# Performance work log

Measured on AMD Instinct MI355X. Metric: run time of the kernel, lower is better.

## Reference

```python
import jax, jax.numpy as jnp
import numpy as np

EMB, NW, H, L, FF, VOCAB, BS = 512, 64, 8, 4, 2048, 50257, 16


def setup_inputs() -> dict:
    key = jax.random.key(0)
    ks = jax.random.split(key, 8)
    d = EMB
    def n(k, shape, s=0.02):
        return jax.random.normal(k, shape, jnp.float32) * s
    return {
        "w_emb": jax.random.normal(ks[0], (BS, NW, d), jnp.float32),
        "table": jax.random.normal(ks[1], (VOCAB, d), jnp.float32) * 0.02,
        "word_enc": n(ks[2], (NW + 1, d)),            # learned token encodings
        "Wqkv": n(ks[3], (L, 3 * d, d)),              # in_proj per layer
        "bqkv": jnp.zeros((L, 3 * d), jnp.float32),
        "Wo": n(ks[4], (L, d, d)),
        "bo": jnp.zeros((L, d), jnp.float32),
        "W1": n(ks[5], (L, FF, d)),
        "b1": jnp.zeros((L, FF), jnp.float32),
        "W2": n(ks[6], (L, d, FF)),
        "b2": jnp.zeros((L, d), jnp.float32),
        "g1": jnp.ones((L, d), jnp.float32),
        "be1": jnp.zeros((L, d), jnp.float32),
        "g2": jnp.ones((L, d), jnp.float32),
        "be2": jnp.zeros((L, d), jnp.float32),
    }


def _ln(x, g, b, eps=1e-5):
    m = x.mean(-1, keepdims=True)
    v = ((x - m) ** 2).mean(-1, keepdims=True)
    return (x - m) * jax.lax.rsqrt(v + eps) * g + b


def reference(w_emb, table, word_enc, Wqkv, bqkv, Wo, bo, W1, b1, W2, b2, g1, be1, g2, be2):
    bs, _, d = w_emb.shape
    dh = d // H
    scale = 1.0 / np.sqrt(dh).astype(np.float32)
    # prepend zero token, add learned encodings -> (bs, NW+1, d)
    x = jnp.concatenate([jnp.zeros((bs, 1, d), w_emb.dtype), w_emb], axis=1) + word_enc
    for l in range(L):
        # self-attention (post-LN TransformerEncoderLayer, ReLU FFN)
        qkv = x @ Wqkv[l].T + bqkv[l]
        q, k, v = jnp.split(qkv, 3, axis=-1)
        s = x.shape[1]
        q = q.reshape(bs, s, H, dh)
        k = k.reshape(bs, s, H, dh)
        v = v.reshape(bs, s, H, dh)
        att = jax.nn.softmax(jnp.einsum('bqhd,bkhd->bhqk', q, k) * scale, axis=-1)
        ctx = jnp.einsum('bhqk,bkhd->bqhd', att, v).reshape(bs, s, d)
        x = _ln(x + ctx @ Wo[l].T + bo[l], g1[l], be1[l])
        h = jax.nn.relu(x @ W1[l].T + b1[l])
        x = _ln(x + h @ W2[l].T + b2[l], g2[l], be2[l])
    out = x[:, :-1]                                   # drop last position -> (bs, NW, d)
    # linear lookup: (out * table).sum(-1) == out @ table.T
    return jnp.einsum('bnd,vd->bnv', out, table)
```

## Files before the change

kernel.cpp:

```cpp
#include <hip/hip_runtime.h>
#include <hip/hip_bf16.h>

#define EMB 512
#define NW  64
#define SEQ 65
#define NH  8
#define DH  64
#define NL  4
#define FF_ 2048
#define VOCAB 50257
#define BS  16
#define TOK (BS*SEQ)
#define TOUT (BS*NW)

typedef short short8  __attribute__((ext_vector_type(8)));
typedef unsigned short ushort8n __attribute__((ext_vector_type(8)));
typedef float f32x4   __attribute__((ext_vector_type(4)));

__device__ __forceinline__ unsigned short f2bf(float f) {
    unsigned u = __float_as_uint(f);
    return (unsigned short)((u + 0x7FFF + ((u >> 16) & 1)) >> 16);
}

template<int N> __device__ __forceinline__ void wait_vm() {
    asm volatile("s_waitcnt vmcnt(%0)" :: "n"(N) : "memory");
}

constexpr int ilog2c(int v) { return v == 32 ? 5 : v == 64 ? 6 : v == 128 ? 7 : 0; }

#define SZ_WQKV (NL*3*EMB*EMB)
#define SZ_WO   (NL*EMB*EMB)
#define SZ_W1   (NL*FF_*EMB)
#define SZ_W2   (NL*EMB*FF_)
#define SZ_TAB  (VOCAB*EMB)
#define CVT_TOTAL (SZ_WQKV+SZ_WO+SZ_W1+SZ_W2+SZ_TAB)
#define O_WO   (SZ_WQKV)
#define O_W1   (O_WO+SZ_WO)
#define O_W2   (O_W1+SZ_W1)
#define O_TAB  (O_W2+SZ_W2)

__global__ void cvt_kernel(const float* __restrict__ wqkv, const float* __restrict__ wo,
                           const float* __restrict__ w1, const float* __restrict__ w2,
                           const float* __restrict__ table, unsigned short* __restrict__ dst) {
    const int U = CVT_TOTAL / 8;
    for (int u = blockIdx.x * blockDim.x + threadIdx.x; u < U; u += gridDim.x * blockDim.x) {
        size_t elem = (size_t)u * 8;
        const float* src; size_t loc = elem;
        if      (elem < O_WO)  { src = wqkv; }
        else if (elem < O_W1)  { src = wo;    loc = elem - O_WO; }
        else if (elem < O_W2)  { src = w1;    loc = elem - O_W1; }
        else if (elem < O_TAB) { src = w2;    loc = elem - O_W2; }
        else                   { src = table; loc = elem - O_TAB; }
        float4 f0 = *(const float4*)(src + loc);
        float4 f1 = *(const float4*)(src + loc + 4);
        ushort8n o;
        o[0]=f2bf(f0.x); o[1]=f2bf(f0.y); o[2]=f2bf(f0.z); o[3]=f2bf(f0.w);
        o[4]=f2bf(f1.x); o[5]=f2bf(f1.y); o[6]=f2bf(f1.z); o[7]=f2bf(f1.w);
        *(ushort8n*)(dst + elem) = o;
    }
}

__global__ void embed_kernel(const float* __restrict__ w_emb,
                             const float* __restrict__ word_enc,
                             float* __restrict__ x32,
                             unsigned short* __restrict__ x16) {
    int idx = blockIdx.x * blockDim.x + threadIdx.x;
    const int total = BS * SEQ * EMB;
    if (idx >= total) return;
    int d = idx & (EMB - 1);
    int s = (idx >> 9) % SEQ;
    int b = idx / (SEQ * EMB);
    float we = word_enc[s * EMB + d];
    float e = (s == 0) ? 0.f : w_emb[((size_t)b * NW + (s - 1)) * EMB + d];
    float v = e + we;
    x32[idx] = v;
    x16[idx] = f2bf(v);
}

template<int TM, int TN, int BK, int OUT_BF16, int RELU, int COMPACT, int SPLITK>
__global__ __launch_bounds__(256) void gemm4(const unsigned short* __restrict__ A,
                                             const unsigned short* __restrict__ B,
                                             const float* __restrict__ bias,
                                             void* __restrict__ C0,
                                             void* __restrict__ C1,
                                             const float* __restrict__ res,
                                             int M, int N, int K, int lda, int ldb) {
    constexpr int LTM = ilog2c(TM);
    constexpr int LTN = ilog2c(TN);
    constexpr int FR  = TM / 32, FC = TN / 32;
    constexpr int WRH = TM / 2,  WCH = TN / 2;
    constexpr int KCH = BK / 32;
    constexpr int AI  = (TM * BK) / (8 * 256);
    constexpr int BI  = (TN * BK) / (8 * 256);
    constexpr int L   = AI + BI;
    constexpr int ASZ = TM * BK * 2;
    constexpr int STRIDE = (TM + TN) * BK * 2;
    __shared__ __align__(16) char smem[3 * STRIDE];

    int t = threadIdx.x;
    int w = t >> 6, l = t & 63;
    int wr = w >> 1, wc = w & 1;
    int lr = l & 15, lh = l >> 4;

    int mtiles = (M + TM - 1) / TM;
    int ntiles = (N + TN - 1) / TN;
    int bid = blockIdx.x;
    int nchunk = gridDim.x >> 3;
    int lin = (bid & 7) * nchunk + (bid >> 3);
    int part = 0;
    if (SPLITK) { int tpp = mtiles * ntiles; part = (lin >= tpp); lin -= part * tpp; }
    int m0 = (lin % mtiles) * TM;
    int n0 = (lin / mtiles) * TN;

    const unsigned short* Ap = A + (size_t)part * K;
    const unsigned short* Bp = B + (size_t)part * K;
    float* Cf = (float*)(part ? C1 : C0);
    const float* biasp = (SPLITK && part) ? nullptr : bias;
    const float* resp  = (SPLITK && part) ? nullptr : res;

    f32x4 acc[FR][FC] = {};
    const int nt = K / BK;

    auto stageA = [&](int kt, int p) {
        char* dst = smem + p * STRIDE;
        #pragma unroll
        for (int i = 0; i < AI; ++i) {
            int tt = i * 256 + t;
            int row = tt & (TM - 1);
            int slot = tt >> LTM;
            int gr = m0 + row;
            if (COMPACT) gr = ((gr >> 6) * SEQ) + (gr & 63);
            else if (gr >= M) gr = M - 1;
            const unsigned short* gp = Ap + (size_t)gr * lda + kt + slot * 8;
            __builtin_amdgcn_global_load_lds(
                (const __attribute__((address_space(1))) void*)gp,
                (__attribute__((address_space(3))) void*)(dst + (size_t)(i * 256 + w * 64) * 16),
                16, 0, 0);
        }
    };
    auto stageB = [&](int kt, int p) {
        char* dst = smem + p * STRIDE + ASZ;
        #pragma unroll
        for (int i = 0; i < BI; ++i) {
            int tt = i * 256 + t;
            int row = tt & (TN - 1);
            int slot = tt >> LTN;
            int gr = n0 + row;
            if (gr >= N) gr = N - 1;
            const unsigned short* gp = Bp + (size_t)gr * ldb + kt + slot * 8;
            __builtin_amdgcn_global_load_lds(
                (const __attribute__((address_space(1))) void*)gp,
                (__attribute__((address_space(3))) void*)(dst + (size_t)(i * 256 + w * 64) * 16),
                16, 0, 0);
        }
    };
    auto compute = [&](int p) {
        const unsigned short* as_ = (const unsigned short*)(smem + p * STRIDE);
        const unsigned short* bs_ = as_ + TM * BK;
        #pragma unroll
        for (int kk = 0; kk < KCH; ++kk) {
            short8 af[FR], bfv[FC];
            #pragma unroll
            for (int mi = 0; mi < FR; ++mi)
                af[mi] = *(const short8*)(as_ + ((size_t)(kk * 4 + lh) * TM + wr * WRH + mi * 16 + lr) * 8);
            #pragma unroll
            for (int ni = 0; ni < FC; ++ni)
                bfv[ni] = *(const short8*)(bs_ + ((size_t)(kk * 4 + lh) * TN + wc * WCH + ni * 16 + lr) * 8);
            #pragma unroll
            for (int mi = 0; mi < FR; ++mi)
                #pragma unroll
                for (int ni = 0; ni < FC; ++ni)
                    acc[mi][ni] = __builtin_amdgcn_mfma_f32_16x16x32_bf16(af[mi], bfv[ni], acc[mi][ni], 0, 0, 0);
        }
    };

    stageA(0, 0); stageB(0, 0);
    if (nt > 1) { stageA(BK, 1); stageB(BK, 1); }

    for (int it = 0; it < nt; ++it) {
        if (it + 1 < nt) wait_vm<L>(); else wait_vm<0>();
        __builtin_amdgcn_s_barrier();
        __builtin_amdgcn_sched_barrier(0);
        if (it + 2 < nt) {
            stageA((it + 2) * BK, (it + 2) % 3);
            stageB((it + 2) * BK, (it + 2) % 3);
        }
        __builtin_amdgcn_s_setprio(1);
        compute(it % 3);
        __builtin_amdgcn_s_setprio(0);
        __builtin_amdgcn_sched_barrier(0);
    }

    if (OUT_BF16) {
        #pragma unroll
        for (int ni = 0; ni < FC; ++ni) {
            int gcol = n0 + wc * WCH + ni * 16 + lr;
            if (gcol >= N) continue;
            float bv = biasp ? biasp[gcol] : 0.f;
            #pragma unroll
            for (int mi = 0; mi < FR; ++mi)
                #pragma unroll
                for (int r = 0; r < 4; ++r) {
                    int grow = m0 + wr * WRH + mi * 16 + lh * 4 + r;
                    if (grow >= M) continue;
                    float v = acc[mi][ni][r] + bv;
                    if (RELU) v = fmaxf(v, 0.f);
                    ((unsigned short*)C0)[(size_t)grow * N + gcol] = f2bf(v);
                }
        }
    } else {
        __syncthreads();
        constexpr int PAD = WCH + 4;
        constexpr int CPR = WCH / 4;
        constexpr int J   = (16 * CPR) / 64;
        float* ep = (float*)smem + (size_t)w * 16 * PAD;
        #pragma unroll
        for (int mi = 0; mi < FR; ++mi) {
            asm volatile("s_waitcnt lgkmcnt(0)" ::: "memory");
            __builtin_amdgcn_sched_barrier(0);
            #pragma unroll
            for (int ni = 0; ni < FC; ++ni)
                #pragma unroll
                for (int r = 0; r < 4; ++r)
                    ep[(lh * 4 + r) * PAD + ni * 16 + lr] = acc[mi][ni][r];
            asm volatile("s_waitcnt lgkmcnt(0)" ::: "memory");
            __builtin_amdgcn_sched_barrier(0);
            #pragma unroll
            for (int j = 0; j < J; ++j) {
                int f4  = j * 64 + l;
                int row = f4 / CPR;
                int c4  = f4 % CPR;
                int grow = m0 + wr * WRH + mi * 16 + row;
                int gc   = n0 + wc * WCH + c4 * 4;
                if (grow < M) {
                    float4 v = *(const float4*)(ep + row * PAD + c4 * 4);
                    if (gc + 3 < N) {
                        if (biasp) {
                            float4 b4 = *(const float4*)(biasp + gc);
                            v.x += b4.x; v.y += b4.y; v.z += b4.z; v.w += b4.w;
                        }
                        if (resp) {
                            const float* rp = resp + (size_t)grow * N + gc;
                            v.x += rp[0]; v.y += rp[1]; v.z += rp[2]; v.w += rp[3];
                        }
                        if (RELU) {
                            v.x = fmaxf(v.x, 0.f); v.y = fmaxf(v.y, 0.f);
                            v.z = fmaxf(v.z, 0.f); v.w = fmaxf(v.w, 0.f);
                        }
                        *(float4*)(Cf + (size_t)grow * N + gc) = v;
                    } else {
                        const float* pv = (const float*)&v;
                        #pragma unroll
                        for (int e = 0; e < 4; ++e)
                            if (gc + e < N) {
                                float vv = pv[e];
                                if (biasp) vv += biasp[gc + e];
                                if (resp)  vv += resp[(size_t)grow * N + gc + e];
                                if (RELU)  vv = fmaxf(vv, 0.f);
                                Cf[(size_t)grow * N + gc + e] = vv;
                            }
                    }
                }
            }
        }
    }
}

template<int TM, int TN, int OUT_BF16, int RELU, int COMPACT>
__global__ __launch_bounds__(256) void gemm2(const unsigned short* __restrict__ A,
                                             const float* __restrict__ B,
                                             const float* __restrict__ bias,
                                             void* __restrict__ C,
                                             int M, int N, int K) {
    constexpr int LTM = (TM == 128) ? 7 : 6;
    constexpr int FR  = TM / 32, FC = TN / 32;
    constexpr int WRH = TM / 2,  WCH = TN / 2;
    constexpr int AI  = TM / 64;
    constexpr int TPR = 256 / TN;
    constexpr int SPT = 4 / TPR;
    constexpr int STRIDE = (TM + TN) * 64;
    __shared__ __align__(16) char smem[2 * STRIDE];

    int t = threadIdx.x;
    int w = t >> 6, l = t & 63;
    int wr = w >> 1, wc = w & 1;
    int lr = l & 15, lh = l >> 4;
    int m0 = blockIdx.y * TM, n0 = blockIdx.x * TN;

    int br = t / TPR, bh = t % TPR;
    int gbr = n0 + br; if (gbr >= N) gbr = N - 1;
    const float* bbase = B + (size_t)gbr * K + bh * (SPT * 8);

    f32x4  acc[FR][FC] = {};
    float4 breg[TN / 32];
    const int nt = K >> 5;

    auto stageA = [&](int kt, int p) {
        char* dst = smem + p * STRIDE;
        #pragma unroll
        for (int i = 0; i < AI; ++i) {
            int tt   = i * 256 + t;
            int row  = tt & (TM - 1);
            int slot = tt >> LTM;
            int gr   = m0 + row;
            if (COMPACT) gr = ((gr >> 6) * SEQ) + (gr & 63);
            else if (gr >= M) gr = M - 1;
            const unsigned short* gp = A + (size_t)gr * K + kt + slot * 8;
            __builtin_amdgcn_global_load_lds(
                (const __attribute__((address_space(1))) void*)gp,
                (__attribute__((address_space(3))) void*)(dst + (size_t)(i * 256 + w * 64) * 16),
                16, 0, 0);
        }
    };
    auto loadB = [&](int kt) {
        const float* bp = bbase + kt;
        #pragma unroll
        for (int j = 0; j < TN / 32; ++j) breg[j] = *(const float4*)(bp + j * 4);
    };
    auto writeB = [&](int p) {
        unsigned short* bs = (unsigned short*)(smem + p * STRIDE + TM * 64);
        #pragma unroll
        for (int s = 0; s < SPT; ++s) {
            ushort8n u;
            #pragma unroll
            for (int e = 0; e < 8; ++e) {
                float f = ((const float*)&breg[s * 2 + (e >> 2)])[e & 3];
                u[e] = f2bf(f);
            }
            int slot = bh * SPT + s;
            *(ushort8n*)(bs + ((size_t)slot * TN + br) * 8) = u;
        }
    };
    auto compute = [&](int p) {
        const unsigned short* as_ = (const unsigned short*)(smem + p * STRIDE);
        const unsigned short* bs_ = as_ + TM * 32;
        short8 af[FR], bfv[FC];
        #pragma unroll
        for (int mi = 0; mi < FR; ++mi)
            af[mi] = *(const short8*)(as_ + ((size_t)lh * TM + wr * WRH + mi * 16 + lr) * 8);
        #pragma unroll
        for (int ni = 0; ni < FC; ++ni)
            bfv[ni] = *(const short8*)(bs_ + ((size_t)lh * TN + wc * WCH + ni * 16 + lr) * 8);
        #pragma unroll
        for (int mi = 0; mi < FR; ++mi)
            #pragma unroll
            for (int ni = 0; ni < FC; ++ni)
                acc[mi][ni] = __builtin_amdgcn_mfma_f32_16x16x32_bf16(af[mi], bfv[ni], acc[mi][ni], 0, 0, 0);
    };

    stageA(0, 0); loadB(0); writeB(0);
    __syncthreads();
    for (int it = 0; it < nt; ++it) {
        int p = it & 1;
        if (it + 1 < nt) { stageA((it + 1) << 5, 1 - p); loadB((it + 1) << 5); }
        compute(p);
        if (it + 1 < nt) writeB(1 - p);
        __syncthreads();
    }

    #pragma unroll
    for (int ni = 0; ni < FC; ++ni) {
        int gcol = n0 + wc * WCH + ni * 16 + lr;
        if (gcol >= N) continue;
        float bv = bias ? bias[gcol] : 0.f;
        #pragma unroll
        for (int mi = 0; mi < FR; ++mi)
            #pragma unroll
            for (int r = 0; r < 4; ++r) {
                int grow = m0 + wr * WRH + mi * 16 + lh * 4 + r;
                if (grow >= M) continue;
                float v = acc[mi][ni][r] + bv;
                if (RELU) v = fmaxf(v, 0.f);
                if (OUT_BF16) ((unsigned short*)C)[(size_t)grow * N + gcol] = f2bf(v);
                else          ((float*)C)[(size_t)grow * N + gcol] = v;
            }
    }
}

#define APAD 65
__global__ __launch_bounds__(256) void attn_fused(const float* __restrict__ qkv,
                                                  unsigned short* __restrict__ ctx16) {
    int qpart = blockIdx.x;
    int h = blockIdx.y, b = blockIdx.z;
    __shared__ float Ks[SEQ * APAD];
    __shared__ float Vs[SEQ * APAD];
    __shared__ float qsh[4][64];
    __shared__ float pws[4][SEQ + 3];

    const float* base = qkv + (size_t)b * SEQ * (3 * EMB) + h * DH;
    int t = threadIdx.x;
    for (int idx = t; idx < SEQ * 16; idx += 256) {
        int r = idx >> 4, c4 = (idx & 15) << 2;
        const float* rp = base + (size_t)r * (3 * EMB);
        float4 kv = *(const float4*)(rp + EMB + c4);
        float4 vv = *(const float4*)(rp + 2 * EMB + c4);
        float* kd = Ks + r * APAD + c4;
        kd[0] = kv.x; kd[1] = kv.y; kd[2] = kv.z; kd[3] = kv.w;
        float* vd = Vs + r * APAD + c4;
        vd[0] = vv.x; vd[1] = vv.y; vd[2] = vv.z; vd[3] = vv.w;
    }
    __syncthreads();

    int w = t >> 6, l = t & 63;
    int qstart = qpart ? 33 : 0;
    int qend   = qpart ? SEQ : 33;
    for (int qi = qstart + w; qi < qend; qi += 4) {
        qsh[w][l] = base[(size_t)qi * (3 * EMB) + l];
        float s = 0.f;
        #pragma unroll 16
        for (int d = 0; d < DH; ++d) s += qsh[w][d] * Ks[l * APAD + d];
        s *= 0.125f;
        float s64 = -1e30f;
        if (l == 0) {
            float acc64 = 0.f;
            #pragma unroll 16
            for (int d = 0; d < DH; ++d) acc64 += qsh[w][d] * Ks[64 * APAD + d];
            s64 = acc64 * 0.125f;
        }
        float m = (l == 0) ? fmaxf(s, s64) : s;
        #pragma unroll
        for (int off = 32; off >= 1; off >>= 1) m = fmaxf(m, __shfl_xor(m, off));
        float e = __expf(s - m);
        pws[w][l] = e;
        float esum = e;
        if (l == 0) { float e64 = __expf(s64 - m); pws[w][64] = e64; esum += e64; }
        #pragma unroll
        for (int off = 32; off >= 1; off >>= 1) esum += __shfl_xor(esum, off);
        float inv = 1.f / esum;
        float acc = 0.f;
        #pragma unroll 13
        for (int j = 0; j < SEQ; ++j) acc += pws[w][j] * Vs[j * APAD + l];
        ctx16[((size_t)b * SEQ + qi) * EMB + h * DH + l] = f2bf(acc * inv);
    }
}

__global__ __launch_bounds__(128) void ln_kernel(const float* __restrict__ x,
                                                 const float* __restrict__ p,
                                                 const float* __restrict__ g,
                                                 const float* __restrict__ be,
                                                 float* __restrict__ y32,
                                                 unsigned short* __restrict__ y16) {
    int row = blockIdx.x;
    int t = threadIdx.x;
    const float4 xv = ((const float4*)(x + (size_t)row * EMB))[t];
    const float4 pv = ((const float4*)(p + (size_t)row * EMB))[t];
    float v0 = xv.x + pv.x, v1 = xv.y + pv.y, v2 = xv.z + pv.z, v3 = xv.w + pv.w;
    float sum = v0 + v1 + v2 + v3;
    float sq  = v0 * v0 + v1 * v1 + v2 * v2 + v3 * v3;
    #pragma unroll
    for (int off = 32; off >= 1; off >>= 1) {
        sum += __shfl_down(sum, off);
        sq  += __shfl_down(sq,  off);
    }
    __shared__ float s0[2], s1[2];
    if ((t & 63) == 0) { s0[t >> 6] = sum; s1[t >> 6] = sq; }
    __syncthreads();
    float S = s0[0] + s0[1], Q = s1[0] + s1[1];
    float mean = S * (1.f / EMB);
    float var  = Q * (1.f / EMB) - mean * mean;
    float rstd = rsqrtf(var + 1e-5f);
    const float4 gv = ((const float4*)g)[t];
    const float4 bv = ((const float4*)be)[t];
    float4 o;
    o.x = (v0 - mean) * rstd * gv.x + bv.x;
    o.y = (v1 - mean) * rstd * gv.y + bv.y;
    o.z = (v2 - mean) * rstd * gv.z + bv.z;
    o.w = (v3 - mean) * rstd * gv.w + bv.w;
    ((float4*)(y32 + (size_t)row * EMB))[t] = o;
    ushort4 h;
    h.x = f2bf(o.x); h.y = f2bf(o.y); h.z = f2bf(o.z); h.w = f2bf(o.w);
    ((ushort4*)(y16 + (size_t)row * EMB))[t] = h;
}

extern "C" void kernel_launch(void* const* d_in, const int* in_sizes, int n_in,
                              void* d_out, int out_size, void* d_ws, size_t ws_size,
                              hipStream_t stream) {
    const float* w_emb    = (const float*)d_in[0];
    const float* table    = (const float*)d_in[1];
    const float* word_enc = (const float*)d_in[2];
    const float* Wqkv     = (const float*)d_in[3];
    const float* bqkv     = (const float*)d_in[4];
    const float* Wo       = (const float*)d_in[5];
    const float* bo       = (const float*)d_in[6];
    const float* W1       = (const float*)d_in[7];
    const float* b1       = (const float*)d_in[8];
    const float* W2       = (const float*)d_in[9];
    const float* b2       = (const float*)d_in[10];
    const float* g1       = (const float*)d_in[11];
    const float* be1      = (const float*)d_in[12];
    const float* g2       = (const float*)d_in[13];
    const float* be2      = (const float*)d_in[14];
    float* out = (float*)d_out;

    const size_t act_bytes = (size_t)TOK * EMB * 4 * 3
                           + (size_t)TOK * 3 * EMB * 4
                           + (size_t)TOK * EMB * 2 * 3
                           + (size_t)TOK * FF_ * 2;
    const size_t wgt_bytes = (size_t)CVT_TOTAL * 2;
    const bool fast = ws_size >= act_bytes + wgt_bytes;

    char* ws = (char*)d_ws;
    unsigned short* wgt16 = nullptr;
    if (fast) { wgt16 = (unsigned short*)ws; ws += wgt_bytes; }
    float* xa32  = (float*)ws;                    ws += (size_t)TOK * EMB * 4;
    float* xb32  = (float*)ws;                    ws += (size_t)TOK * EMB * 4;
    float* qkv32 = (float*)ws;                    ws += (size_t)TOK * 3 * EMB * 4;
    float* proj32= (float*)ws;                    ws += (size_t)TOK * EMB * 4;
    unsigned short* hbuf16= (unsigned short*)ws;  ws += (size_t)TOK * FF_ * 2;
    unsigned short* xa16  = (unsigned short*)ws;  ws += (size_t)TOK * EMB * 2;
    unsigned short* xb16  = (unsigned short*)ws;  ws += (size_t)TOK * EMB * 2;
    unsigned short* ctx16 = (unsigned short*)ws;  ws += (size_t)TOK * EMB * 2;
    float* projb  = qkv32;

    if (fast) cvt_kernel<<<2048, 256, 0, stream>>>(Wqkv, Wo, W1, W2, table, wgt16);

    {
        int total = BS * SEQ * EMB;
        embed_kernel<<<(total + 255) / 256, 256, 0, stream>>>(w_emb, word_enc, xa32, xa16);
    }

    if (fast) {
        const unsigned short* wq16 = wgt16;
        const unsigned short* wo16 = wgt16 + O_WO;
        const unsigned short* w116 = wgt16 + O_W1;
        const unsigned short* w216 = wgt16 + O_W2;
        const unsigned short* tab16= wgt16 + O_TAB;

        for (int l = 0; l < NL; ++l) {
            gemm4<64,32,64,0,0,0,0><<<dim3(816), 256, 0, stream>>>(
                xa16, wq16 + (size_t)l * 3 * EMB * EMB, bqkv + (size_t)l * 3 * EMB,
                qkv32, nullptr, nullptr, TOK, 3 * EMB, EMB, EMB, EMB);
            attn_fused<<<dim3(2, NH, BS), 256, 0, stream>>>(qkv32, ctx16);
            gemm4<64,32,64,0,0,0,1><<<dim3(544), 256, 0, stream>>>(
                ctx16, wo16 + (size_t)l * EMB * EMB, bo + (size_t)l * EMB,
                proj32, projb, xa32, TOK, EMB, 256, EMB, EMB);
            ln_kernel<<<TOK, 128, 0, stream>>>(proj32, projb,
                g1 + (size_t)l * EMB, be1 + (size_t)l * EMB, xb32, xb16);
            gemm4<64,32,64,1,1,0,0><<<dim3(1088), 256, 0, stream>>>(
                xb16, w116 + (size_t)l * FF_ * EMB, b1 + (size_t)l * FF_,
                hbuf16, nullptr, nullptr, TOK, FF_, EMB, EMB, EMB);
            gemm4<64,32,64,0,0,0,1><<<dim3(544), 256, 0, stream>>>(
                hbuf16, w216 + (size_t)l * EMB * FF_, b2 + (size_t)l * EMB,
                proj32, projb, xb32, TOK, EMB, 1024, FF_, FF_);
            ln_kernel<<<TOK, 128, 0, stream>>>(proj32, projb,
                g2 + (size_t)l * EMB, be2 + (size_t)l * EMB, xa32, xa16);
        }
        gemm4<64,128,32,0,0,1,0><<<dim3(6288), 256, 0, stream>>>(
            xa16, tab16, nullptr, out, nullptr, nullptr, TOUT, VOCAB, EMB, EMB, EMB);
    } else {
        for (int l = 0; l < NL; ++l) {
            const float* Wqkv_l = Wqkv + (size_t)l * 3 * EMB * EMB;
            const float* Wo_l   = Wo   + (size_t)l * EMB * EMB;
            const float* W1_l   = W1   + (size_t)l * FF_ * EMB;
            const float* W2_l   = W2   + (size_t)l * EMB * FF_;
            gemm2<64,64,0,0,0><<<dim3((3 * EMB) / 64, (TOK + 63) / 64), 256, 0, stream>>>(
                xa16, Wqkv_l, bqkv + (size_t)l * 3 * EMB, qkv32, TOK, 3 * EMB, EMB);
            attn_fused<<<dim3(2, NH, BS), 256, 0, stream>>>(qkv32, ctx16);
            gemm2<64,64,0,0,0><<<dim3(EMB / 64, (TOK + 63) / 64), 256, 0, stream>>>(
                ctx16, Wo_l, bo + (size_t)l * EMB, proj32, TOK, EMB, EMB);
            ln_kernel<<<TOK, 128, 0, stream>>>(xa32, proj32, g1 + (size_t)l * EMB, be1 + (size_t)l * EMB, xb32, xb16);
            gemm2<64,64,1,1,0><<<dim3(FF_ / 64, (TOK + 63) / 64), 256, 0, stream>>>(
                xb16, W1_l, b1 + (size_t)l * FF_, hbuf16, TOK, FF_, EMB);
            gemm2<64,64,0,0,0><<<dim3(EMB / 64, (TOK + 63) / 64), 256, 0, stream>>>(
                hbuf16, W2_l, b2 + (size_t)l * EMB, proj32, TOK, EMB, FF_);
            ln_kernel<<<TOK, 128, 0, stream>>>(xb32, proj32, g2 + (size_t)l * EMB, be2 + (size_t)l * EMB, xa32, xa16);
        }
        gemm2<128,128,0,0,1><<<dim3((VOCAB + 127) / 128, TOUT / 128), 256, 0, stream>>>(
            xa16, table, nullptr, out, TOUT, VOCAB, EMB);
    }
}
```

Measured before the change: 575.5 us.

## Fuse layer GEMMs with bias/residual/LayerNorm via direct-load full-row dgemm

```diff
diff --git a/kernel.cpp b/kernel.cpp
--- a/kernel.cpp
+++ b/kernel.cpp
@@ -12,6 +12,7 @@
 #define BS  16
 #define TOK (BS*SEQ)
 #define TOUT (BS*NW)
+#define MT32 ((TOK + 31) / 32)
 
 typedef short short8  __attribute__((ext_vector_type(8)));
 typedef unsigned short ushort8n __attribute__((ext_vector_type(8)));
@@ -77,14 +78,147 @@
     x16[idx] = f2bf(v);
 }
 
-template<int TM, int TN, int BK, int OUT_BF16, int RELU, int COMPACT, int SPLITK>
+template<int K, int MODE>
+__global__ __launch_bounds__(512) void dgemm(const unsigned short* __restrict__ A,
+                                             const unsigned short* __restrict__ B,
+                                             const float* __restrict__ bias,
+                                             const float* __restrict__ res,
+                                             const float* __restrict__ g,
+                                             const float* __restrict__ be,
+                                             float* __restrict__ out32,
+                                             unsigned short* __restrict__ out16,
+                                             int M, int N) {
+    int t = threadIdx.x, w = t >> 6, l = t & 63;
+    int lr = l & 15, lh = l >> 4;
+    int bid = blockIdx.x;
+    int mt = bid % MT32, ns = bid / MT32;
+    int m0 = mt * 32;
+    int c0 = ns * 512 + w * 64;
+
+    int ar0 = m0 + lr;       if (ar0 >= M) ar0 = M - 1;
+    int ar1 = m0 + 16 + lr;  if (ar1 >= M) ar1 = M - 1;
+    const unsigned short* a0 = A + (size_t)ar0 * K + lh * 8;
+    const unsigned short* a1 = A + (size_t)ar1 * K + lh * 8;
+    const unsigned short* bb = B + (size_t)(c0 + lr) * K + lh * 8;
+
+    f32x4 acc[2][4] = {};
+    #pragma unroll 2
+    for (int k0 = 0; k0 < K; k0 += 32) {
+        short8 af0 = *(const short8*)(a0 + k0);
+        short8 af1 = *(const short8*)(a1 + k0);
+        short8 bfv[4];
+        #pragma unroll
+        for (int ni = 0; ni < 4; ++ni)
+            bfv[ni] = *(const short8*)(bb + (size_t)ni * 16 * K + k0);
+        #pragma unroll
+        for (int ni = 0; ni < 4; ++ni) {
+            acc[0][ni] = __builtin_amdgcn_mfma_f32_16x16x32_bf16(af0, bfv[ni], acc[0][ni], 0, 0, 0);
+            acc[1][ni] = __builtin_amdgcn_mfma_f32_16x16x32_bf16(af1, bfv[ni], acc[1][ni], 0, 0, 0);
+        }
+    }
+
+    if (MODE == 2) {
+        __shared__ float sred[32][8], qred[32][8], mstat[32], rstat[32];
+        float vals[2][4][4];
+        float bv[4];
+        #pragma unroll
+        for (int ni = 0; ni < 4; ++ni) bv[ni] = bias[c0 + ni * 16 + lr];
+        float ps[2][4] = {}, pq[2][4] = {};
+        #pragma unroll
+        for (int mi = 0; mi < 2; ++mi)
+            #pragma unroll
+            for (int r = 0; r < 4; ++r) {
+                int row = m0 + mi * 16 + lh * 4 + r;
+                int rc = row < M ? row : M - 1;
+                #pragma unroll
+                for (int ni = 0; ni < 4; ++ni) {
+                    float v = acc[mi][ni][r] + bv[ni] + res[(size_t)rc * 512 + c0 + ni * 16 + lr];
+                    vals[mi][ni][r] = v;
+                    ps[mi][r] += v;
+                    pq[mi][r] += v * v;
+                }
+            }
+        #pragma unroll
+        for (int off = 8; off >= 1; off >>= 1)
+            #pragma unroll
+            for (int mi = 0; mi < 2; ++mi)
+                #pragma unroll
+                for (int r = 0; r < 4; ++r) {
+                    ps[mi][r] += __shfl_xor(ps[mi][r], off);
+                    pq[mi][r] += __shfl_xor(pq[mi][r], off);
+                }
+        if (lr == 0) {
+            #pragma unroll
+            for (int mi = 0; mi < 2; ++mi)
+                #pragma unroll
+                for (int r = 0; r < 4; ++r) {
+                    sred[mi * 16 + lh * 4 + r][w] = ps[mi][r];
+                    qred[mi * 16 + lh * 4 + r][w] = pq[mi][r];
+                }
+        }
+        __syncthreads();
+        if (t < 32) {
+            float S = 0.f, Q = 0.f;
+            #pragma unroll
+            for (int j = 0; j < 8; ++j) { S += sred[t][j]; Q += qred[t][j]; }
+            float mean = S * (1.f / 512.f);
+            float var  = Q * (1.f / 512.f) - mean * mean;
+            mstat[t] = mean;
+            rstat[t] = rsqrtf(var + 1e-5f);
+        }
+        __syncthreads();
+        float gv[4], bev[4];
+        #pragma unroll
+        for (int ni = 0; ni < 4; ++ni) {
+            gv[ni] = g[c0 + ni * 16 + lr];
+            bev[ni] = be[c0 + ni * 16 + lr];
+        }
+        #pragma unroll
+        for (int mi = 0; mi < 2; ++mi)
+            #pragma unroll
+            for (int r = 0; r < 4; ++r) {
+                int lrow = mi * 16 + lh * 4 + r;
+                int row = m0 + lrow;
+                if (row >= M) continue;
+                float mean = mstat[lrow], rstd = rstat[lrow];
+                #pragma unroll
+                for (int ni = 0; ni < 4; ++ni) {
+                    int col = c0 + ni * 16 + lr;
+                    float o = (vals[mi][ni][r] - mean) * rstd * gv[ni] + bev[ni];
+                    out32[(size_t)row * 512 + col] = o;
+                    out16[(size_t)row * 512 + col] = f2bf(o);
+                }
+            }
+    } else {
+        float bv[4];
+        #pragma unroll
+        for (int ni = 0; ni < 4; ++ni) bv[ni] = bias ? bias[c0 + ni * 16 + lr] : 0.f;
+        #pragma unroll
+        for (int mi = 0; mi < 2; ++mi)
+            #pragma unroll
+            for (int r = 0; r < 4; ++r) {
+                int row = m0 + mi * 16 + lh * 4 + r;
+                if (row >= M) continue;
+                #pragma unroll
+                for (int ni = 0; ni < 4; ++ni) {
+                    int col = c0 + ni * 16 + lr;
+                    float v = acc[mi][ni][r] + bv[ni];
+                    if (MODE == 1) {
+                        v = fmaxf(v, 0.f);
+                        out16[(size_t)row * N + col] = f2bf(v);
+                    } else {
+                        out32[(size_t)row * N + col] = v;
+                    }
+                }
+            }
+    }
+}
+
+template<int TM, int TN, int BK, int COMPACT>
 __global__ __launch_bounds__(256) void gemm4(const unsigned short* __restrict__ A,
                                              const unsigned short* __restrict__ B,
-                                             const float* __restrict__ bias,
-                                             void* __restrict__ C0,
-                                             void* __restrict__ C1,
-                                             const float* __restrict__ res,
-                                             int M, int N, int K, int lda, int ldb) {
+                                             float* __restrict__ C,
+                                             int M, int N, int K) {
     constexpr int LTM = ilog2c(TM);
     constexpr int LTN = ilog2c(TN);
     constexpr int FR  = TM / 32, FC = TN / 32;
@@ -103,20 +237,11 @@
     int lr = l & 15, lh = l >> 4;
 
     int mtiles = (M + TM - 1) / TM;
-    int ntiles = (N + TN - 1) / TN;
     int bid = blockIdx.x;
     int nchunk = gridDim.x >> 3;
     int lin = (bid & 7) * nchunk + (bid >> 3);
-    int part = 0;
-    if (SPLITK) { int tpp = mtiles * ntiles; part = (lin >= tpp); lin -= part * tpp; }
     int m0 = (lin % mtiles) * TM;
     int n0 = (lin / mtiles) * TN;
-
-    const unsigned short* Ap = A + (size_t)part * K;
-    const unsigned short* Bp = B + (size_t)part * K;
-    float* Cf = (float*)(part ? C1 : C0);
-    const float* biasp = (SPLITK && part) ? nullptr : bias;
-    const float* resp  = (SPLITK && part) ? nullptr : res;
 
     f32x4 acc[FR][FC] = {};
     const int nt = K / BK;
@@ -131,7 +256,7 @@
             int gr = m0 + row;
             if (COMPACT) gr = ((gr >> 6) * SEQ) + (gr & 63);
             else if (gr >= M) gr = M - 1;
-            const unsigned short* gp = Ap + (size_t)gr * lda + kt + slot * 8;
+            const unsigned short* gp = A + (size_t)gr * K + kt + slot * 8;
             __builtin_amdgcn_global_load_lds(
                 (const __attribute__((address_space(1))) void*)gp,
                 (__attribute__((address_space(3))) void*)(dst + (size_t)(i * 256 + w * 64) * 16),
@@ -147,7 +272,7 @@
             int slot = tt >> LTN;
             int gr = n0 + row;
             if (gr >= N) gr = N - 1;
-            const unsigned short* gp = Bp + (size_t)gr * ldb + kt + slot * 8;
+            const unsigned short* gp = B + (size_t)gr * K + kt + slot * 8;
             __builtin_amdgcn_global_load_lds(
                 (const __attribute__((address_space(1))) void*)gp,
                 (__attribute__((address_space(3))) void*)(dst + (size_t)(i * 256 + w * 64) * 16),
@@ -191,75 +316,38 @@
         __builtin_amdgcn_sched_barrier(0);
     }
 
-    if (OUT_BF16) {
-        #pragma unroll
-        for (int ni = 0; ni < FC; ++ni) {
-            int gcol = n0 + wc * WCH + ni * 16 + lr;
-            if (gcol >= N) continue;
-            float bv = biasp ? biasp[gcol] : 0.f;
-            #pragma unroll
-            for (int mi = 0; mi < FR; ++mi)
-                #pragma unroll
-                for (int r = 0; r < 4; ++r) {
-                    int grow = m0 + wr * WRH + mi * 16 + lh * 4 + r;
-                    if (grow >= M) continue;
-                    float v = acc[mi][ni][r] + bv;
-                    if (RELU) v = fmaxf(v, 0.f);
-                    ((unsigned short*)C0)[(size_t)grow * N + gcol] = f2bf(v);
-                }
-        }
-    } else {
-        __syncthreads();
-        constexpr int PAD = WCH + 4;
-        constexpr int CPR = WCH / 4;
-        constexpr int J   = (16 * CPR) / 64;
-        float* ep = (float*)smem + (size_t)w * 16 * PAD;
-        #pragma unroll
-        for (int mi = 0; mi < FR; ++mi) {
-            asm volatile("s_waitcnt lgkmcnt(0)" ::: "memory");
-            __builtin_amdgcn_sched_barrier(0);
-            #pragma unroll
-            for (int ni = 0; ni < FC; ++ni)
-                #pragma unroll
-                for (int r = 0; r < 4; ++r)
-                    ep[(lh * 4 + r) * PAD + ni * 16 + lr] = acc[mi][ni][r];
-            asm volatile("s_waitcnt lgkmcnt(0)" ::: "memory");
-            __builtin_amdgcn_sched_barrier(0);
-            #pragma unroll
-            for (int j = 0; j < J; ++j) {
-                int f4  = j * 64 + l;
-                int row = f4 / CPR;
-                int c4  = f4 % CPR;
-                int grow = m0 + wr * WRH + mi * 16 + row;
-                int gc   = n0 + wc * WCH + c4 * 4;
-                if (grow < M) {
-                    float4 v = *(const float4*)(ep + row * PAD + c4 * 4);
-                    if (gc + 3 < N) {
-                        if (biasp) {
-                            float4 b4 = *(const float4*)(biasp + gc);
-                            v.x += b4.x; v.y += b4.y; v.z += b4.z; v.w += b4.w;
-                        }
-                        if (resp) {
-                            const float* rp = resp + (size_t)grow * N + gc;
-                            v.x += rp[0]; v.y += rp[1]; v.z += rp[2]; v.w += rp[3];
-                        }
-                        if (RELU) {
-                            v.x = fmaxf(v.x, 0.f); v.y = fmaxf(v.y, 0.f);
-                            v.z = fmaxf(v.z, 0.f); v.w = fmaxf(v.w, 0.f);
-                        }
-                        *(float4*)(Cf + (size_t)grow * N + gc) = v;
-                    } else {
-                        const float* pv = (const float*)&v;
-                        #pragma unroll
-                        for (int e = 0; e < 4; ++e)
-                            if (gc + e < N) {
-                                float vv = pv[e];
-                                if (biasp) vv += biasp[gc + e];
-                                if (resp)  vv += resp[(size_t)grow * N + gc + e];
-                                if (RELU)  vv = fmaxf(vv, 0.f);
-                                Cf[(size_t)grow * N + gc + e] = vv;
-                            }
-                    }
+    __syncthreads();
+    constexpr int PAD = WCH + 4;
+    constexpr int CPR = WCH / 4;
+    constexpr int J   = (16 * CPR) / 64;
+    float* ep = (float*)smem + (size_t)w * 16 * PAD;
+    #pragma unroll
+    for (int mi = 0; mi < FR; ++mi) {
+        asm volatile("s_waitcnt lgkmcnt(0)" ::: "memory");
+        __builtin_amdgcn_sched_barrier(0);
+        #pragma unroll
+        for (int ni = 0; ni < FC; ++ni)
+            #pragma unroll
+            for (int r = 0; r < 4; ++r)
+                ep[(lh * 4 + r) * PAD + ni * 16 + lr] = acc[mi][ni][r];
+        asm volatile("s_waitcnt lgkmcnt(0)" ::: "memory");
+        __builtin_amdgcn_sched_barrier(0);
+        #pragma unroll
+        for (int j = 0; j < J; ++j) {
+            int f4  = j * 64 + l;
+            int row = f4 / CPR;
+            int c4  = f4 % CPR;
+            int grow = m0 + wr * WRH + mi * 16 + row;
+            int gc   = n0 + wc * WCH + c4 * 4;
+            if (grow < M) {
+                float4 v = *(const float4*)(ep + row * PAD + c4 * 4);
+                if (gc + 3 < N) {
+                    *(float4*)(C + (size_t)grow * N + gc) = v;
+                } else {
+                    const float* pv = (const float*)&v;
+                    #pragma unroll
+                    for (int e = 0; e < 4; ++e)
+                        if (gc + e < N) C[(size_t)grow * N + gc + e] = pv[e];
                 }
             }
         }
@@ -510,7 +598,6 @@
     unsigned short* xa16  = (unsigned short*)ws;  ws += (size_t)TOK * EMB * 2;
     unsigned short* xb16  = (unsigned short*)ws;  ws += (size_t)TOK * EMB * 2;
     unsigned short* ctx16 = (unsigned short*)ws;  ws += (size_t)TOK * EMB * 2;
-    float* projb  = qkv32;
 
     if (fast) cvt_kernel<<<2048, 256, 0, stream>>>(Wqkv, Wo, W1, W2, table, wgt16);
 
@@ -527,26 +614,24 @@
         const unsigned short* tab16= wgt16 + O_TAB;
 
         for (int l = 0; l < NL; ++l) {
-            gemm4<64,32,64,0,0,0,0><<<dim3(816), 256, 0, stream>>>(
+            dgemm<EMB,0><<<dim3(MT32 * 3), 512, 0, stream>>>(
                 xa16, wq16 + (size_t)l * 3 * EMB * EMB, bqkv + (size_t)l * 3 * EMB,
-                qkv32, nullptr, nullptr, TOK, 3 * EMB, EMB, EMB, EMB);
+                nullptr, nullptr, nullptr, qkv32, nullptr, TOK, 3 * EMB);
             attn_fused<<<dim3(2, NH, BS), 256, 0, stream>>>(qkv32, ctx16);
-            gemm4<64,32,64,0,0,0,1><<<dim3(544), 256, 0, stream>>>(
+            dgemm<EMB,2><<<dim3(MT32), 512, 0, stream>>>(
                 ctx16, wo16 + (size_t)l * EMB * EMB, bo + (size_t)l * EMB,
-                proj32, projb, xa32, TOK, EMB, 256, EMB, EMB);
-            ln_kernel<<<TOK, 128, 0, stream>>>(proj32, projb,
-                g1 + (size_t)l * EMB, be1 + (size_t)l * EMB, xb32, xb16);
-            gemm4<64,32,64,1,1,0,0><<<dim3(1088), 256, 0, stream>>>(
+                xa32, g1 + (size_t)l * EMB, be1 + (size_t)l * EMB,
+                xb32, xb16, TOK, EMB);
+            dgemm<EMB,1><<<dim3(MT32 * 4), 512, 0, stream>>>(
                 xb16, w116 + (size_t)l * FF_ * EMB, b1 + (size_t)l * FF_,
-                hbuf16, nullptr, nullptr, TOK, FF_, EMB, EMB, EMB);
-            gemm4<64,32,64,0,0,0,1><<<dim3(544), 256, 0, stream>>>(
+                nullptr, nullptr, nullptr, nullptr, hbuf16, TOK, FF_);
+            dgemm<FF_,2><<<dim3(MT32), 512, 0, stream>>>(
                 hbuf16, w216 + (size_t)l * EMB * FF_, b2 + (size_t)l * EMB,
-                proj32, projb, xb32, TOK, EMB, 1024, FF_, FF_);
-            ln_kernel<<<TOK, 128, 0, stream>>>(proj32, projb,
-                g2 + (size_t)l * EMB, be2 + (size_t)l * EMB, xa32, xa16);
-        }
-        gemm4<64,128,32,0,0,1,0><<<dim3(6288), 256, 0, stream>>>(
-            xa16, tab16, nullptr, out, nullptr, nullptr, TOUT, VOCAB, EMB, EMB, EMB);
+                xb32, g2 + (size_t)l * EMB, be2 + (size_t)l * EMB,
+                xa32, xa16, TOK, EMB);
+        }
+        gemm4<128,128,32,1><<<dim3(3144), 256, 0, stream>>>(
+            xa16, tab16, out, TOUT, VOCAB, EMB);
     } else {
         for (int l = 0; l < NL; ++l) {
             const float* Wqkv_l = Wqkv + (size_t)l * 3 * EMB * EMB;
```

New measurement: 922.6 us. +60.3%, slower.
